# Kernel tuning notes

Hardware: AMD Instinct MI355X
Metric: run time of the kernel (lower is better)

The kernel has to match this reference:

```python
import jax, jax.numpy as jnp
import numpy as np
from jax import lax

D_MODEL = 2048
D_STATE = 16
D_CONV = 4
B_SZ = 2
T_LEN = 2048


def setup_inputs() -> dict:
    key = jax.random.key(0)
    ks = jax.random.split(key, 8)
    x = jax.random.normal(ks[0], (B_SZ, T_LEN, D_MODEL), dtype=jnp.float32)
    h = jnp.zeros((B_SZ, D_MODEL, D_STATE), dtype=jnp.float32)
    norm_w = jnp.ones((D_MODEL,), dtype=jnp.float32)
    in_proj_w = jax.random.normal(ks[1], (2 * D_MODEL, D_MODEL), dtype=jnp.float32) * (D_MODEL ** -0.5)
    conv_w = jax.random.normal(ks[2], (D_MODEL, 1, D_CONV), dtype=jnp.float32) * 0.5
    conv_b = jnp.zeros((D_MODEL,), dtype=jnp.float32)
    x_proj_w = jax.random.normal(ks[3], (D_MODEL + 2 * D_STATE, D_MODEL), dtype=jnp.float32) * (D_MODEL ** -0.5)
    A_log = jnp.broadcast_to(jnp.log(jnp.arange(1, D_STATE + 1, dtype=jnp.float32))[None, :], (D_MODEL, D_STATE)).copy()
    D = jnp.ones((D_MODEL,), dtype=jnp.float32)
    out_proj_w = jax.random.normal(ks[4], (D_MODEL, D_MODEL), dtype=jnp.float32) * (D_MODEL ** -0.5)
    return {"x": x, "h": h, "norm_w": norm_w, "in_proj_w": in_proj_w,
            "conv_w": conv_w, "conv_b": conv_b, "x_proj_w": x_proj_w,
            "A_log": A_log, "D": D, "out_proj_w": out_proj_w}


def _rmsnorm(x, w, eps=1e-6):
    ms = jnp.mean(jnp.square(x.astype(jnp.float32)), axis=-1, keepdims=True)
    return (x * lax.rsqrt(ms + eps).astype(x.dtype)) * w.astype(x.dtype)


def reference(x, h, norm_w, in_proj_w, conv_w, conv_b, x_proj_w, A_log, D, out_proj_w):
    B, T, d_model = x.shape
    d_state = A_log.shape[1]
    residual = x
    x_normed = _rmsnorm(x, norm_w)
    xz = x_normed @ in_proj_w.T                      # (B, T, 2*d_model)
    x_branch, z = jnp.split(xz, 2, axis=-1)
    # depthwise causal conv1d: torch pads both sides by d_conv-1 then slices [:T],
    # equivalent to left-pad-only causal conv.
    xc = x_branch.transpose(0, 2, 1)                 # (B, d_model, T)
    xc = lax.conv_general_dilated(
        xc, conv_w, window_strides=(1,), padding=[(D_CONV - 1, 0)],
        dimension_numbers=("NCH", "OIH", "NCH"), feature_group_count=d_model)
    xc = xc + conv_b[None, :, None]
    x_ssm = jax.nn.silu(xc.transpose(0, 2, 1))       # (B, T, d_model)

    # SSM core
    proj = x_ssm @ x_proj_w.T                        # (B, T, d_model + 2*d_state)
    delta_raw = proj[..., :d_model]
    B_in = proj[..., d_model:d_model + d_state]
    C_in = proj[..., d_model + d_state:]
    delta = jax.nn.softplus(delta_raw)               # (B, T, d_model)
    A = -jnp.exp(A_log.astype(jnp.float32))          # (d_model, d_state)

    def step(h_c, inp):
        d_t, b_t, c_t, x_t = inp                     # (B,dm) (B,ds) (B,ds) (B,dm)
        A_bar = jnp.exp(d_t[:, :, None] * A[None])   # (B, dm, ds)
        h_c = A_bar * h_c + (d_t * x_t)[:, :, None] * b_t[:, None, :]
        y_t = jnp.einsum("bdn,bn->bd", h_c, c_t) + D * x_t
        return h_c, y_t

    xs = (delta.transpose(1, 0, 2), B_in.transpose(1, 0, 2),
          C_in.transpose(1, 0, 2), x_ssm.transpose(1, 0, 2))
    h_new, ys = lax.scan(step, h.astype(x.dtype), xs)
    y = ys.transpose(1, 0, 2)                        # (B, T, d_model)

    y = y * jax.nn.silu(z)
    out = residual + y @ out_proj_w.T
    return out, lax.stop_gradient(h_new)
```

## Files before the change

### kernel.cpp

```cpp
#include <hip/hip_runtime.h>
#include <cstdint>
#include <cstddef>


typedef __bf16 bf16_t;
typedef __attribute__((ext_vector_type(8))) __bf16 bf16x8;
typedef __attribute__((ext_vector_type(4))) __bf16 bf16x4;
typedef __attribute__((ext_vector_type(4))) float f32x4;

#define D_MODEL 2048
#define D_STATE 16
#define B_SZ 2
#define T_LEN 2048
#define N_ROWS (B_SZ * T_LEN)
#define N_PAD  2304
#define N_CHUNK 32
#define L_CHUNK (T_LEN / N_CHUNK)
#define LOG2E 1.4426950408889634f

__device__ __forceinline__ void load_lds16(const void* g, void* l) {
    __builtin_amdgcn_global_load_lds(
        (const __attribute__((address_space(1))) void*)(uintptr_t)g,
        (__attribute__((address_space(3))) void*)(uintptr_t)l,
        16, 0, 0);
}

#define VMW(n) asm volatile("s_waitcnt vmcnt(" #n ")" ::: "memory")
#define BAR()  do { __builtin_amdgcn_s_barrier(); __builtin_amdgcn_sched_barrier(0); } while (0)

__global__ __launch_bounds__(256) void cast_w13(
    const float* __restrict__ w1, const float* __restrict__ w3,
    bf16_t* __restrict__ d1, bf16_t* __restrict__ d3)
{
    int i = blockIdx.x * 256 + threadIdx.x;
    const int n1 = 4096 * 2048 / 4;
    if (i < n1) {
        f32x4 v = ((const f32x4*)w1)[i];
        ((bf16x4*)d1)[i] = __builtin_convertvector(v, bf16x4);
    } else {
        int j = i - n1;
        f32x4 v = ((const f32x4*)w3)[j];
        ((bf16x4*)d3)[j] = __builtin_convertvector(v, bf16x4);
    }
}

__global__ __launch_bounds__(256) void cast_pad_w2(
    const float* __restrict__ s, bf16_t* __restrict__ d)
{
    int i = blockIdx.x * 256 + threadIdx.x;
    int row = i >> 11;
    int col = i & 2047;
    float v = (row < 2080) ? s[(size_t)row * 2048 + col] : 0.f;
    d[i] = (bf16_t)v;
}

__global__ __launch_bounds__(256) void rmsnorm_kernel(
    const float* __restrict__ x, const float* __restrict__ w,
    bf16_t* __restrict__ xn)
{
    int row = blockIdx.x;
    int tid = threadIdx.x;
    const f32x4* xr = (const f32x4*)(x + (size_t)row * D_MODEL);
    f32x4 v0 = xr[tid];
    f32x4 v1 = xr[tid + 256];
    float ss = 0.f;
    #pragma unroll
    for (int e = 0; e < 4; ++e) { ss = fmaf(v0[e], v0[e], ss); ss = fmaf(v1[e], v1[e], ss); }
    #pragma unroll
    for (int o = 32; o > 0; o >>= 1) ss += __shfl_down(ss, o, 64);
    __shared__ float red[4];
    if ((tid & 63) == 0) red[tid >> 6] = ss;
    __syncthreads();
    float tot = red[0] + red[1] + red[2] + red[3];
    float scale = rsqrtf(tot * (1.f / D_MODEL) + 1e-6f);
    const f32x4* w4 = (const f32x4*)w;
    f32x4 m0 = v0 * w4[tid] * scale;
    f32x4 m1 = v1 * w4[tid + 256] * scale;
    bf16x4* xo = (bf16x4*)(xn + (size_t)row * D_MODEL);
    xo[tid]       = __builtin_convertvector(m0, bf16x4);
    xo[tid + 256] = __builtin_convertvector(m1, bf16x4);
}

template<int MODE>
__global__ __launch_bounds__(512, 2) void gemm_bt(
    const bf16_t* __restrict__ A, const bf16_t* __restrict__ Bw, int K,
    float* __restrict__ out0, bf16_t* __restrict__ out1,
    const float* __restrict__ add)
{
    __shared__ __align__(16) char smem[131072];
    char* const ldsA = smem;
    char* const ldsB = smem + 65536;

    const int tid  = threadIdx.x;
    const int bm   = blockIdx.x, bn = blockIdx.y;
    const int lane = tid & 63;
    const int wave = tid >> 6;
    const int wm   = wave >> 2;
    const int wn   = wave & 3;
    const int fr   = lane & 15;
    const int quad = lane >> 4;

    const int rS   = tid >> 2;
    const int cS   = tid & 3;
    const int gcol = ((cS - ((rS >> 1) & 3)) & 3) * 8;
    const bf16_t* sA0 = A  + (size_t)(bm * 256 + rS) * K + gcol;
    const bf16_t* sA1 = sA0 + (size_t)128 * K;
    const bf16_t* sB0 = Bw + (size_t)(bn * 256 + rS) * K + gcol;
    const bf16_t* sB1 = sB0 + (size_t)128 * K;

    const int swz  = ((quad + ((fr >> 1) & 3)) & 3) * 8;
    const int aOff = (wm * 128 + fr) * 32 + swz;
    const int bOff = (wn * 64  + fr) * 32 + swz;

    f32x4 acc[8][4];
    #pragma unroll
    for (int i = 0; i < 8; ++i)
        #pragma unroll
        for (int j = 0; j < 4; ++j) acc[i][j] = {0.f, 0.f, 0.f, 0.f};

#define STAGE(b) do { \
        load_lds16(sA0, ldsA + (b) * 16384 + tid * 16);        \
        load_lds16(sA1, ldsA + (b) * 16384 + tid * 16 + 8192); \
        load_lds16(sB0, ldsB + (b) * 16384 + tid * 16);        \
        load_lds16(sB1, ldsB + (b) * 16384 + tid * 16 + 8192); \
        sA0 += 32; sA1 += 32; sB0 += 32; sB1 += 32; } while (0)

    auto compute = [&](int cb) {
        const bf16_t* pA = (const bf16_t*)(ldsA + cb * 16384);
        const bf16_t* pB = (const bf16_t*)(ldsB + cb * 16384);
        bf16x8 bfr[4];
        #pragma unroll
        for (int j = 0; j < 4; ++j)
            bfr[j] = *(const bf16x8*)(pB + bOff + j * 512);
        __builtin_amdgcn_s_setprio(1);
        #pragma unroll
        for (int i = 0; i < 8; ++i) {
            bf16x8 a = *(const bf16x8*)(pA + aOff + i * 512);
            #pragma unroll
            for (int j = 0; j < 4; ++j)
                acc[i][j] = __builtin_amdgcn_mfma_f32_16x16x32_bf16(
                    a, bfr[j], acc[i][j], 0, 0, 0);
        }
        __builtin_amdgcn_s_setprio(0);
    };

    const int nt = K >> 5;
    STAGE(0); STAGE(1); STAGE(2);
    for (int t = 0; t < nt - 3; ++t) {
        VMW(8); BAR();
        STAGE((t + 3) & 3);
        compute(t & 3);
    }
    VMW(8); BAR(); compute((nt - 3) & 3);
    VMW(4); BAR(); compute((nt - 2) & 3);
    VMW(0); BAR(); compute((nt - 1) & 3);
#undef STAGE

    float* const cs = (float*)smem;
    __syncthreads();
    for (int s = 0; s < 4; ++s) {
        if (wm == (s >> 1)) {
            const int i0 = (s & 1) * 4;
            #pragma unroll
            for (int ii = 0; ii < 4; ++ii)
                #pragma unroll
                for (int j = 0; j < 4; ++j)
                    #pragma unroll
                    for (int rr = 0; rr < 4; ++rr)
                        cs[(ii * 16 + quad * 4 + rr) * 268 + wn * 64 + j * 16 + fr]
                            = acc[i0 + ii][j][rr];
        }
        __syncthreads();
        #pragma unroll
        for (int k = 0; k < 8; ++k) {
            const int idx = tid + k * 512;
            const int row = idx >> 6;
            const int c4  = (idx & 63) << 2;
            f32x4 v = *(const f32x4*)(cs + row * 268 + c4);
            const int gr = bm * 256 + s * 64 + row;
            const int gc = bn * 256 + c4;
            if (MODE == 0) {
                if (bn < 8) {
                    *(f32x4*)&out0[(size_t)gr * 2048 + gc] = v;
                } else {
                    bf16x4 o;
                    #pragma unroll
                    for (int e = 0; e < 4; ++e) {
                        float sv = v[e];
                        o[e] = (bf16_t)(sv / (1.f + __expf(-sv)));
                    }
                    *(bf16x4*)&out1[(size_t)gr * 2048 + (gc - 2048)] = o;
                }
            } else if (MODE == 1) {
                if (bn < 8) {
                    #pragma unroll
                    for (int e = 0; e < 4; ++e) {
                        float sv = v[e];
                        v[e] = fmaxf(sv, 0.f) + __logf(1.f + __expf(-fabsf(sv)));
                    }
                }
                *(f32x4*)&out0[(size_t)gr * N_PAD + gc] = v;
            } else {
                f32x4 a4 = *(const f32x4*)&add[(size_t)gr * 2048 + gc];
                *(f32x4*)&out0[(size_t)gr * 2048 + gc] = v + a4;
            }
        }
        __syncthreads();
    }
}

__global__ __launch_bounds__(256) void conv_silu_kernel(
    const float* __restrict__ xb, const float* __restrict__ cw,
    const float* __restrict__ cb, bf16_t* __restrict__ xs_b)
{
    int id = blockIdx.x * 256 + threadIdx.x;
    int d  = id & 2047;
    int tb = (id >> 11) & 255;
    int b  = id >> 19;
    float w0 = cw[d * 4 + 0], w1 = cw[d * 4 + 1], w2 = cw[d * 4 + 2], w3 = cw[d * 4 + 3];
    float bias = cb[d];
    int t0 = tb * 8;
    size_t base = (size_t)b * T_LEN;
    float v[11];
    #pragma unroll
    for (int i = 0; i < 11; ++i) {
        int t = t0 - 3 + i;
        v[i] = (t >= 0) ? xb[(base + t) * 2048 + d] : 0.f;
    }
    #pragma unroll
    for (int j = 0; j < 8; ++j) {
        float s = bias + w0 * v[j] + w1 * v[j + 1] + w2 * v[j + 2] + w3 * v[j + 3];
        float sl = s / (1.f + __expf(-s));
        xs_b[(base + t0 + j) * D_MODEL + d] = (bf16_t)sl;
    }
}

#define PF 4

__global__ __launch_bounds__(256) void scan_phase1(
    const float* __restrict__ proj, const bf16_t* __restrict__ xs,
    const float* __restrict__ A_log,
    float* __restrict__ Aprod, float* __restrict__ hfin)
{
    int wi   = blockIdx.x * 4 + (threadIdx.x >> 6);
    int lane = threadIdx.x & 63;
    int nq   = lane & 3;
    int dsub = lane >> 2;
    int c  = wi & 31;
    int dg = (wi >> 5) & 127;
    int b  = wi >> 12;
    int dd = dg * 16 + dsub;

    float A2[4], h[4], Ap[4];
    #pragma unroll
    for (int j = 0; j < 4; ++j) {
        A2[j] = -__expf(A_log[dd * D_STATE + nq * 4 + j]) * LOG2E;
        h[j] = 0.f; Ap[j] = 1.f;
    }
    const int t0 = c * L_CHUNK;
    const int tmax = t0 + L_CHUNK - 1;

    float p_da[PF], p_xv[PF];
    f32x4 p_B[PF];
    #pragma unroll
    for (int u = 0; u < PF; ++u) {
        size_t row = (size_t)b * T_LEN + t0 + u;
        const float* pr = proj + row * N_PAD;
        p_da[u] = pr[dd];
        p_xv[u] = (float)xs[row * D_MODEL + dd];
        p_B[u]  = *(const f32x4*)(pr + D_MODEL + nq * 4);
    }

    for (int it = 0; it < L_CHUNK; it += PF) {
        #pragma unroll
        for (int u = 0; u < PF; ++u) {
            int t = t0 + it + u;
            float da = p_da[u], xv = p_xv[u];
            f32x4 Bv = p_B[u];
            int tn = t + PF; tn = (tn > tmax) ? tmax : tn;
            {
                size_t row = (size_t)b * T_LEN + tn;
                const float* pr = proj + row * N_PAD;
                p_da[u] = pr[dd];
                p_xv[u] = (float)xs[row * D_MODEL + dd];
                p_B[u]  = *(const f32x4*)(pr + D_MODEL + nq * 4);
            }
            float dx = da * xv;
            #pragma unroll
            for (int j = 0; j < 4; ++j) {
                float a = exp2f(da * A2[j]);
                Ap[j] *= a;
                h[j] = fmaf(a, h[j], dx * Bv[j]);
            }
        }
    }
    size_t o = ((size_t)c * 4096 + b * 2048 + dd) * D_STATE + nq * 4;
    *(f32x4*)(Aprod + o) = f32x4{Ap[0], Ap[1], Ap[2], Ap[3]};
    *(f32x4*)(hfin  + o) = f32x4{h[0], h[1], h[2], h[3]};
}

__global__ __launch_bounds__(256) void scan_phase2(
    const float* __restrict__ h_in, const float* __restrict__ Aprod,
    float* __restrict__ hfin, float* __restrict__ h_out)
{
    int g = blockIdx.x * 256 + threadIdx.x;
    float h = h_in[g];
    for (int c = 0; c < N_CHUNK; ++c) {
        size_t o = (size_t)c * 65536 + g;
        float a   = Aprod[o];
        float loc = hfin[o];
        hfin[o] = h;
        h = fmaf(a, h, loc);
    }
    h_out[g] = h;
}

__global__ __launch_bounds__(256) void scan_phase3(
    const float* __restrict__ proj, const bf16_t* __restrict__ xs,
    const bf16_t* __restrict__ zg, const float* __restrict__ A_log,
    const float* __restrict__ Dv, const float* __restrict__ hinit,
    bf16_t* __restrict__ yg)
{
    int wi   = blockIdx.x * 4 + (threadIdx.x >> 6);
    int lane = threadIdx.x & 63;
    int nq   = lane & 3;
    int dsub = lane >> 2;
    int c  = wi & 31;
    int dg = (wi >> 5) & 127;
    int b  = wi >> 12;
    int dd = dg * 16 + dsub;

    float A2[4], h[4];
    size_t o = ((size_t)c * 4096 + b * 2048 + dd) * D_STATE + nq * 4;
    #pragma unroll
    for (int j = 0; j < 4; ++j) {
        A2[j] = -__expf(A_log[dd * D_STATE + nq * 4 + j]) * LOG2E;
        h[j]  = hinit[o + j];
    }
    float Dd = Dv[dd];
    const int t0 = c * L_CHUNK;
    const int tmax = t0 + L_CHUNK - 1;

    float p_da[PF], p_xv[PF], p_sz[PF];
    f32x4 p_B[PF], p_C[PF];
    #pragma unroll
    for (int u = 0; u < PF; ++u) {
        size_t row = (size_t)b * T_LEN + t0 + u;
        const float* pr = proj + row * N_PAD;
        p_da[u] = pr[dd];
        p_xv[u] = (float)xs[row * D_MODEL + dd];
        p_sz[u] = (float)zg[row * 2048 + dd];
        p_B[u]  = *(const f32x4*)(pr + D_MODEL + nq * 4);
        p_C[u]  = *(const f32x4*)(pr + D_MODEL + D_STATE + nq * 4);
    }

    for (int it = 0; it < L_CHUNK; it += PF) {
        #pragma unroll
        for (int u = 0; u < PF; ++u) {
            int t = t0 + it + u;
            float da = p_da[u], xv = p_xv[u], sz = p_sz[u];
            f32x4 Bv = p_B[u], Cv = p_C[u];
            int tn = t + PF; tn = (tn > tmax) ? tmax : tn;
            {
                size_t row = (size_t)b * T_LEN + tn;
                const float* pr = proj + row * N_PAD;
                p_da[u] = pr[dd];
                p_xv[u] = (float)xs[row * D_MODEL + dd];
                p_sz[u] = (float)zg[row * 2048 + dd];
                p_B[u]  = *(const f32x4*)(pr + D_MODEL + nq * 4);
                p_C[u]  = *(const f32x4*)(pr + D_MODEL + D_STATE + nq * 4);
            }
            float dx = da * xv;
            float yp = 0.f;
            #pragma unroll
            for (int j = 0; j < 4; ++j) {
                float a = exp2f(da * A2[j]);
                h[j] = fmaf(a, h[j], dx * Bv[j]);
                yp = fmaf(h[j], Cv[j], yp);
            }
            yp += __shfl_xor(yp, 1, 64);
            yp += __shfl_xor(yp, 2, 64);
            if (nq == 0) {
                float y = fmaf(Dd, xv, yp);
                yg[((size_t)b * T_LEN + t) * D_MODEL + dd] = (bf16_t)(y * sz);
            }
        }
    }
}

extern "C" void kernel_launch(void* const* d_in, const int* in_sizes, int n_in,
                              void* d_out, int out_size, void* d_ws, size_t ws_size,
                              hipStream_t stream)
{
    const float* x    = (const float*)d_in[0];
    const float* h0   = (const float*)d_in[1];
    const float* nw   = (const float*)d_in[2];
    const float* w_in = (const float*)d_in[3];
    const float* cw   = (const float*)d_in[4];
    const float* cb   = (const float*)d_in[5];
    const float* w_x  = (const float*)d_in[6];
    const float* alog = (const float*)d_in[7];
    const float* dv   = (const float*)d_in[8];
    const float* w_out= (const float*)d_in[9];
    float* out  = (float*)d_out;
    float* hout = out + (size_t)N_ROWS * D_MODEL;

    char* ws = (char*)d_ws;
    size_t off = 0;
    auto alloc = [&](size_t bytes) -> void* {
        void* p = ws + off;
        off += (bytes + 255) & ~(size_t)255;
        return p;
    };
    bf16_t* W1  = (bf16_t*)alloc((size_t)4096 * 2048 * 2);
    bf16_t* W2  = (bf16_t*)alloc((size_t)N_PAD * 2048 * 2);
    bf16_t* W3  = (bf16_t*)alloc((size_t)2048 * 2048 * 2);
    bf16_t* XN  = (bf16_t*)alloc((size_t)N_ROWS * 2048 * 2);
    float*  XB  = (float*) alloc((size_t)N_ROWS * 2048 * 4);
    bf16_t* ZG  = (bf16_t*)alloc((size_t)N_ROWS * 2048 * 2);
    float*  PROJ= (float*) alloc((size_t)N_ROWS * N_PAD * 4);
    float* APROD= (float*) alloc((size_t)N_CHUNK * 4096 * D_STATE * 4);
    float* HFIN = (float*) alloc((size_t)N_CHUNK * 4096 * D_STATE * 4);
    bf16_t* XSb = W1;
    bf16_t* YG  = XN;

    cast_w13<<<(4096 * 2048 / 4 + 2048 * 2048 / 4) / 256, 256, 0, stream>>>(w_in, w_out, W1, W3);
    cast_pad_w2<<<(N_PAD * 2048) / 256, 256, 0, stream>>>(w_x, W2);

    rmsnorm_kernel<<<N_ROWS, 256, 0, stream>>>(x, nw, XN);
    gemm_bt<0><<<dim3(16, 16), 512, 0, stream>>>(XN, W1, 2048, XB, ZG, nullptr);
    conv_silu_kernel<<<(B_SZ * (T_LEN / 8) * D_MODEL) / 256, 256, 0, stream>>>(XB, cw, cb, XSb);
    gemm_bt<1><<<dim3(16, N_PAD / 256), 512, 0, stream>>>(XSb, W2, 2048, PROJ, nullptr, nullptr);
    scan_phase1<<<2048, 256, 0, stream>>>(PROJ, XSb, alog, APROD, HFIN);
    scan_phase2<<<256, 256, 0, stream>>>(h0, APROD, HFIN, hout);
    scan_phase3<<<2048, 256, 0, stream>>>(PROJ, XSb, ZG, alog, dv, HFIN, YG);
    gemm_bt<2><<<dim3(16, 8), 512, 0, stream>>>(YG, W3, 2048, out, nullptr, x);

    (void)in_sizes; (void)n_in; (void)out_size; (void)ws_size;
}
```

Baseline: 531.0 us.

## Interleave LDS prefetch with MFMA phases and remap workgroups for locality

Splits each K-tile's compute into four phases, each issuing one async global-to-LDS load and a barrier before its MFMAs, so loads and matrix ops interleave at finer grain. It also remaps the linear block index with a stride-of-8 permutation into (bm, bn) with bm taken from the low 4 bits, presumably to spread or group tiles across XCDs for better L2 reuse. The extra per-phase barriers add sync cost. The remap hardcodes 16 M-tiles, which breaks for GEMMs with a different grid shape.

Result: no change. 536.5 us (+1.0%).

```diff
diff --git a/kernel.cpp b/kernel.cpp
--- a/kernel.cpp
+++ b/kernel.cpp
@@ -92,7 +92,12 @@
     char* const ldsB = smem + 65536;
 
     const int tid  = threadIdx.x;
-    const int bm   = blockIdx.x, bn = blockIdx.y;
+    const int nwg = gridDim.x * gridDim.y;
+    const int lin = blockIdx.x + gridDim.x * blockIdx.y;
+    const int wg  = (lin & 7) * (nwg >> 3) + (lin >> 3);
+    const int bm  = wg & 15;
+    const int bn  = wg >> 4;
+
     const int lane = tid & 63;
     const int wave = tid >> 6;
     const int wm   = wave >> 2;
@@ -118,43 +123,62 @@
         #pragma unroll
         for (int j = 0; j < 4; ++j) acc[i][j] = {0.f, 0.f, 0.f, 0.f};
 
-#define STAGE(b) do { \
-        load_lds16(sA0, ldsA + (b) * 16384 + tid * 16);        \
-        load_lds16(sA1, ldsA + (b) * 16384 + tid * 16 + 8192); \
-        load_lds16(sB0, ldsB + (b) * 16384 + tid * 16);        \
-        load_lds16(sB1, ldsB + (b) * 16384 + tid * 16 + 8192); \
-        sA0 += 32; sA1 += 32; sB0 += 32; sB1 += 32; } while (0)
-
-    auto compute = [&](int cb) {
-        const bf16_t* pA = (const bf16_t*)(ldsA + cb * 16384);
-        const bf16_t* pB = (const bf16_t*)(ldsB + cb * 16384);
-        bf16x8 bfr[4];
-        #pragma unroll
-        for (int j = 0; j < 4; ++j)
-            bfr[j] = *(const bf16x8*)(pB + bOff + j * 512);
-        __builtin_amdgcn_s_setprio(1);
-        #pragma unroll
-        for (int i = 0; i < 8; ++i) {
-            bf16x8 a = *(const bf16x8*)(pA + aOff + i * 512);
-            #pragma unroll
-            for (int j = 0; j < 4; ++j)
-                acc[i][j] = __builtin_amdgcn_mfma_f32_16x16x32_bf16(
-                    a, bfr[j], acc[i][j], 0, 0, 0);
-        }
-        __builtin_amdgcn_s_setprio(0);
-    };
+#define SL0(b) load_lds16(sA0, ldsA + (b) * 16384 + tid * 16)
+#define SL1(b) load_lds16(sA1, ldsA + (b) * 16384 + tid * 16 + 8192)
+#define SL2(b) load_lds16(sB0, ldsB + (b) * 16384 + tid * 16)
+#define SL3(b) load_lds16(sB1, ldsB + (b) * 16384 + tid * 16 + 8192)
+#define ADV()  do { sA0 += 32; sA1 += 32; sB0 += 32; sB1 += 32; } while (0)
+
+#define PHASE(cb, p, SLX)                                                     \
+    {                                                                         \
+        const bf16_t* pA = (const bf16_t*)(ldsA + (cb) * 16384);              \
+        bf16x8 aLo = *(const bf16x8*)(pA + aOff + (2 * (p)) * 512);           \
+        bf16x8 aHi = *(const bf16x8*)(pA + aOff + (2 * (p) + 1) * 512);       \
+        SLX;                                                                  \
+        BAR();                                                                \
+        __builtin_amdgcn_s_setprio(1);                                        \
+        _Pragma("unroll")                                                     \
+        for (int j = 0; j < 4; ++j)                                           \
+            acc[2 * (p)][j] = __builtin_amdgcn_mfma_f32_16x16x32_bf16(        \
+                aLo, bfr[j], acc[2 * (p)][j], 0, 0, 0);                       \
+        _Pragma("unroll")                                                     \
+        for (int j = 0; j < 4; ++j)                                           \
+            acc[2 * (p) + 1][j] = __builtin_amdgcn_mfma_f32_16x16x32_bf16(    \
+                aHi, bfr[j], acc[2 * (p) + 1][j], 0, 0, 0);                   \
+        __builtin_amdgcn_s_setprio(0);                                        \
+    }
+
+#define TILE(cb, nb, ST)                                                      \
+    {                                                                         \
+        const bf16_t* pB = (const bf16_t*)(ldsB + (cb) * 16384);              \
+        bf16x8 bfr[4];                                                        \
+        _Pragma("unroll")                                                     \
+        for (int j = 0; j < 4; ++j)                                           \
+            bfr[j] = *(const bf16x8*)(pB + bOff + j * 512);                   \
+        PHASE(cb, 0, if (ST) SL0(nb))                                         \
+        PHASE(cb, 1, if (ST) SL1(nb))                                         \
+        PHASE(cb, 2, if (ST) SL2(nb))                                         \
+        PHASE(cb, 3, if (ST) { SL3(nb); ADV(); })                             \
+    }
 
     const int nt = K >> 5;
-    STAGE(0); STAGE(1); STAGE(2);
+    SL0(0); SL1(0); SL2(0); SL3(0); ADV();
+    SL0(1); SL1(1); SL2(1); SL3(1); ADV();
+    SL0(2); SL1(2); SL2(2); SL3(2); ADV();
     for (int t = 0; t < nt - 3; ++t) {
         VMW(8); BAR();
-        STAGE((t + 3) & 3);
-        compute(t & 3);
-    }
-    VMW(8); BAR(); compute((nt - 3) & 3);
-    VMW(4); BAR(); compute((nt - 2) & 3);
-    VMW(0); BAR(); compute((nt - 1) & 3);
-#undef STAGE
+        TILE(t & 3, (t + 3) & 3, true)
+    }
+    VMW(8); BAR(); TILE((nt - 3) & 3, 0, false)
+    VMW(4); BAR(); TILE((nt - 2) & 3, 0, false)
+    VMW(0); BAR(); TILE((nt - 1) & 3, 0, false)
+#undef SL0
+#undef SL1
+#undef SL2
+#undef SL3
+#undef ADV
+#undef PHASE
+#undef TILE
 
     float* const cs = (float*)smem;
     __syncthreads();
```
